# Performance work log

Hardware: AMD Instinct MI355X
Metric: run time of the kernel (lower is better)

Reference implementation:

```python
import jax, jax.numpy as jnp
import numpy as np

H = 8      # head_nums
D = 64     # head_planes
SCALE = D ** -0.5


def setup_inputs() -> dict:
    key = jax.random.key(0)
    ks = jax.random.split(key, 7)
    B, Nq, Nkv = 2, 2048, 2048
    Cq, Ck, I = 1024, 768, H * D
    return {
        "x": jax.random.normal(ks[0], (B, Nq, Cq), jnp.float32),
        "context": jax.random.normal(ks[1], (B, Nkv, Ck), jnp.float32),
        "Wq": jax.random.normal(ks[2], (Cq, I), jnp.float32) * (Cq ** -0.5),
        "Wk": jax.random.normal(ks[3], (Ck, I), jnp.float32) * (Ck ** -0.5),
        "Wv": jax.random.normal(ks[4], (Ck, I), jnp.float32) * (Ck ** -0.5),
        "Wo": jax.random.normal(ks[5], (I, Cq), jnp.float32) * (I ** -0.5),
        "bo": jnp.zeros((Cq,), jnp.float32),
    }


def reference(x, context, Wq, Wk, Wv, Wo, bo):
    B, Nq, _ = x.shape
    Nkv = context.shape[1]
    # projections (bias-free, as in to_q/to_k/to_v)
    q = (x @ Wq).reshape(B, Nq, H, D)        # b i h d
    k = (context @ Wk).reshape(B, Nkv, H, D)  # b j h d
    v = (context @ Wv).reshape(B, Nkv, H, D)
    # scaled dot-product attention, full [B,H,Nq,Nkv] scores as in original
    sim = jnp.einsum('bihd,bjhd->bhij', q, k) * SCALE
    attn = jax.nn.softmax(sim, axis=-1)
    out = jnp.einsum('bhij,bjhd->bihd', attn, v).reshape(B, Nq, H * D)
    # to_out linear (dropout_prob=0.0 -> identity)
    return out @ Wo + bo
```

## Files before the change

### kernel.cpp

```cpp
#include <hip/hip_runtime.h>
#include <hip/hip_bf16.h>

typedef __hip_bfloat16 bf16;
typedef __attribute__((ext_vector_type(8))) short short8;
typedef __attribute__((ext_vector_type(4))) float f32x4;

#define MFMA16(a, b, c) __builtin_amdgcn_mfma_f32_16x16x32_bf16((a), (b), (c), 0, 0, 0)

#define BATCH 2
#define NQ 2048
#define NKV 2048
#define HEADS 8
#define DHEAD 64
#define CQ 1024
#define CK 768
#define IDIM 512
#define SCALE 0.125f

__device__ __forceinline__ short8 ld8(const bf16* p) {
    return *(const short8*)p;
}

__device__ __forceinline__ void async_ld16(const bf16* g, bf16* l) {
    __builtin_amdgcn_global_load_lds((__attribute__((address_space(1))) const void*)g,
                                     (__attribute__((address_space(3))) void*)l,
                                     16, 0, 0);
}

__global__ __launch_bounds__(256) void prologue(
    const float* __restrict__ x, const float* __restrict__ ctx,
    const float* __restrict__ Wq, const float* __restrict__ Wk,
    const float* __restrict__ Wv, const float* __restrict__ Wo,
    bf16* __restrict__ Xb, bf16* __restrict__ Cb,
    bf16* __restrict__ WqT, bf16* __restrict__ WkT,
    bf16* __restrict__ WvT, bf16* __restrict__ WoT) {
    __shared__ float tile[64][65];
    const int t = threadIdx.x;
    const int bx = blockIdx.x;

    if (bx < 3584) {
        int idx = bx * 256 + t;
        const int NX8 = (4096 * 1024) / 8;
        const float4* srcp;
        bf16* dstp;
        if (idx < NX8) {
            srcp = (const float4*)x + (size_t)idx * 2;
            dstp = Xb + (size_t)idx * 8;
        } else {
            int j = idx - NX8;
            srcp = (const float4*)ctx + (size_t)j * 2;
            dstp = Cb + (size_t)j * 8;
        }
        float4 v0 = srcp[0], v1 = srcp[1];
        bf16 tmp[8] = {__float2bfloat16(v0.x), __float2bfloat16(v0.y),
                       __float2bfloat16(v0.z), __float2bfloat16(v0.w),
                       __float2bfloat16(v1.x), __float2bfloat16(v1.y),
                       __float2bfloat16(v1.z), __float2bfloat16(v1.w)};
        *(short8*)dstp = *(short8*)tmp;
        return;
    }

    int tb = bx - 3584;
    const float* src; bf16* dst; int R, C, ti;
    if (tb < 128)      { src = Wq; dst = WqT; R = 1024; C = 512;  ti = tb; }
    else if (tb < 224) { src = Wk; dst = WkT; R = 768;  C = 512;  ti = tb - 128; }
    else if (tb < 320) { src = Wv; dst = WvT; R = 768;  C = 512;  ti = tb - 224; }
    else               { src = Wo; dst = WoT; R = 512;  C = 1024; ti = tb - 320; }
    const int tilesC = C >> 6;
    const int tr = ti / tilesC, tc = ti - tr * tilesC;

    {
        int row = t >> 4;
        int c4 = (t & 15) * 4;
#pragma unroll
        for (int p = 0; p < 4; ++p) {
            float4 v = *(const float4*)&src[(size_t)(tr * 64 + p * 16 + row) * C + tc * 64 + c4];
            tile[p * 16 + row][c4 + 0] = v.x;
            tile[p * 16 + row][c4 + 1] = v.y;
            tile[p * 16 + row][c4 + 2] = v.z;
            tile[p * 16 + row][c4 + 3] = v.w;
        }
    }
    __syncthreads();
    {
        int oc = t >> 2;
        int r0 = (t & 3) * 16;
        bf16 tmp[16];
#pragma unroll
        for (int j = 0; j < 16; ++j)
            tmp[j] = __float2bfloat16(tile[r0 + j][oc]);
        bf16* dp = dst + (size_t)(tc * 64 + oc) * R + tr * 64 + r0;
        *(short8*)dp = *(short8*)&tmp[0];
        *(short8*)(dp + 8) = *(short8*)&tmp[8];
    }
}

__global__ __launch_bounds__(256) void qkv_gemm(
    const bf16* __restrict__ Xb, const bf16* __restrict__ Cb,
    const bf16* __restrict__ WqT, const bf16* __restrict__ WkT,
    const bf16* __restrict__ WvT,
    bf16* __restrict__ Qb, bf16* __restrict__ Kb, bf16* __restrict__ Vt) {
    __shared__ bf16 At[2][64 * 64];
    __shared__ bf16 Bts[2][128 * 64];

    const int z = blockIdx.z;
    const bf16* A  = (z == 0) ? Xb : Cb;
    const bf16* Bt = (z == 0) ? WqT : (z == 1) ? WkT : WvT;
    const int K = (z == 0) ? 1024 : 768;

    const int t = threadIdx.x;
    const int wave = t >> 6;
    const int lane = t & 63;
    const int n15 = lane & 15;
    const int quad = lane >> 4;
    const int wm = wave >> 1;
    const int wn = wave & 1;
    const int bm = blockIdx.y;
    const int bn = blockIdx.x;

    f32x4 acc[2][4] = {};

    const bf16* Ablk = A + (size_t)bm * 64 * K;
    const bf16* Bblk = Bt + (size_t)bn * 128 * K;

    int ar[2], ac[2], br[4], bc[4];
#pragma unroll
    for (int i = 0; i < 2; ++i) {
        int g = i * 256 + t;
        ar[i] = g >> 3; ac[i] = ((g & 7) ^ (ar[i] & 7)) * 8;
    }
#pragma unroll
    for (int i = 0; i < 4; ++i) {
        int g = i * 256 + t;
        br[i] = g >> 3; bc[i] = ((g & 7) ^ (br[i] & 7)) * 8;
    }

#pragma unroll
    for (int i = 0; i < 2; ++i)
        async_ld16(Ablk + ar[i] * K + ac[i], &At[0][(i * 256 + t) * 8]);
#pragma unroll
    for (int i = 0; i < 4; ++i)
        async_ld16(Bblk + br[i] * K + bc[i], &Bts[0][(i * 256 + t) * 8]);
    __syncthreads();

    for (int k0 = 0; k0 < K; k0 += 64) {
        const int p = (k0 >> 6) & 1;
        if (k0 + 64 < K) {
            const int q = p ^ 1;
            const int kn = k0 + 64;
#pragma unroll
            for (int i = 0; i < 2; ++i)
                async_ld16(Ablk + ar[i] * K + kn + ac[i], &At[q][(i * 256 + t) * 8]);
#pragma unroll
            for (int i = 0; i < 4; ++i)
                async_ld16(Bblk + br[i] * K + kn + bc[i], &Bts[q][(i * 256 + t) * 8]);
        }

#pragma unroll
        for (int kh = 0; kh < 2; ++kh) {
            short8 af[2], bfr[4];
#pragma unroll
            for (int mt = 0; mt < 2; ++mt) {
                int R = wm * 32 + mt * 16 + n15;
                af[mt] = ld8(&At[p][R * 64 + (((kh * 4 + quad) ^ (R & 7)) * 8)]);
            }
#pragma unroll
            for (int nt = 0; nt < 4; ++nt) {
                int R = wn * 64 + nt * 16 + n15;
                bfr[nt] = ld8(&Bts[p][R * 64 + (((kh * 4 + quad) ^ (R & 7)) * 8)]);
            }
#pragma unroll
            for (int mt = 0; mt < 2; ++mt)
#pragma unroll
                for (int nt = 0; nt < 4; ++nt)
                    acc[mt][nt] = MFMA16(af[mt], bfr[nt], acc[mt][nt]);
        }

        __syncthreads();
    }

    bf16* C = (z == 0) ? Qb : (z == 1) ? Kb : Vt;
#pragma unroll
    for (int mt = 0; mt < 2; ++mt) {
#pragma unroll
        for (int nt = 0; nt < 4; ++nt) {
            int col = bn * 128 + wn * 64 + nt * 16 + n15;
#pragma unroll
            for (int r = 0; r < 4; ++r) {
                int row = bm * 64 + wm * 32 + mt * 16 + quad * 4 + r;
                bf16 v = __float2bfloat16(acc[mt][nt][r]);
                if (z < 2) {
                    C[(size_t)row * 512 + col] = v;
                } else {
                    int b = row >> 11, j = row & 2047;
                    int h = col >> 6, d = col & 63;
                    C[(size_t)(((b << 3) + h) * 64 + d) * 2048 + j] = v;
                }
            }
        }
    }
}

__global__ __launch_bounds__(256) void out_gemm(const bf16* __restrict__ A,
                                                const bf16* __restrict__ Bt,
                                                const float* __restrict__ bias,
                                                float* __restrict__ C) {
    const int K = 512, N = 1024;
    __shared__ char SMEM[49152];
    bf16* At  = (bf16*)SMEM;
    bf16* Bts = (bf16*)(SMEM + 16384);
    float* Ep = (float*)SMEM;

    const int t = threadIdx.x;
    const int wave = t >> 6;
    const int lane = t & 63;
    const int n15 = lane & 15;
    const int quad = lane >> 4;
    const int wm = wave >> 1;
    const int wn = wave & 1;
    const int bm = blockIdx.y;
    const int bn = blockIdx.x;

    f32x4 acc[2][4] = {};

    const bf16* Ablk = A + (size_t)bm * 64 * K;
    const bf16* Bblk = Bt + (size_t)bn * 128 * K;

    int ar[2], ac[2], br[4], bc[4];
#pragma unroll
    for (int i = 0; i < 2; ++i) {
        int g = i * 256 + t;
        ar[i] = g >> 3; ac[i] = ((g & 7) ^ (ar[i] & 7)) * 8;
    }
#pragma unroll
    for (int i = 0; i < 4; ++i) {
        int g = i * 256 + t;
        br[i] = g >> 3; bc[i] = ((g & 7) ^ (br[i] & 7)) * 8;
    }

#pragma unroll
    for (int i = 0; i < 2; ++i)
        async_ld16(Ablk + ar[i] * K + ac[i], At + (i * 256 + t) * 8);
#pragma unroll
    for (int i = 0; i < 4; ++i)
        async_ld16(Bblk + br[i] * K + bc[i], Bts + (i * 256 + t) * 8);
    __syncthreads();

    for (int k0 = 0; k0 < K; k0 += 64) {
        const int p = (k0 >> 6) & 1;
        if (k0 + 64 < K) {
            const int q = p ^ 1;
            const int kn = k0 + 64;
#pragma unroll
            for (int i = 0; i < 2; ++i)
                async_ld16(Ablk + ar[i] * K + kn + ac[i], At + q * 4096 + (i * 256 + t) * 8);
#pragma unroll
            for (int i = 0; i < 4; ++i)
                async_ld16(Bblk + br[i] * K + kn + bc[i], Bts + q * 8192 + (i * 256 + t) * 8);
        }

#pragma unroll
        for (int kh = 0; kh < 2; ++kh) {
            short8 af[2], bfr[4];
#pragma unroll
            for (int mt = 0; mt < 2; ++mt) {
                int R = wm * 32 + mt * 16 + n15;
                af[mt] = ld8(At + p * 4096 + R * 64 + (((kh * 4 + quad) ^ (R & 7)) * 8));
            }
#pragma unroll
            for (int nt = 0; nt < 4; ++nt) {
                int R = wn * 64 + nt * 16 + n15;
                bfr[nt] = ld8(Bts + p * 8192 + R * 64 + (((kh * 4 + quad) ^ (R & 7)) * 8));
            }
#pragma unroll
            for (int mt = 0; mt < 2; ++mt)
#pragma unroll
                for (int nt = 0; nt < 4; ++nt)
                    acc[mt][nt] = MFMA16(af[mt], bfr[nt], acc[mt][nt]);
        }

        __syncthreads();
    }

#pragma unroll
    for (int mt = 0; mt < 2; ++mt)
#pragma unroll
        for (int nt = 0; nt < 4; ++nt) {
            int col = wn * 64 + nt * 16 + n15;
#pragma unroll
            for (int r = 0; r < 4; ++r) {
                int row = wm * 32 + mt * 16 + quad * 4 + r;
                Ep[row * 132 + col] = acc[mt][nt][r];
            }
        }
    __syncthreads();

#pragma unroll
    for (int i = 0; i < 8; ++i) {
        int f4 = i * 256 + t;
        int row = f4 >> 5;
        int c4 = (f4 & 31) * 4;
        float4 v = *(float4*)&Ep[row * 132 + c4];
        float4 bv = *(const float4*)&bias[bn * 128 + c4];
        v.x += bv.x; v.y += bv.y; v.z += bv.z; v.w += bv.w;
        *(float4*)&C[(size_t)(bm * 64 + row) * N + bn * 128 + c4] = v;
    }
}

__global__ __launch_bounds__(512, 1) void flash_attn(const bf16* __restrict__ Q,
                                                     const bf16* __restrict__ K,
                                                     const bf16* __restrict__ Vt,
                                                     bf16* __restrict__ O) {
    __shared__ bf16 Kt[2][64 * 64];
    __shared__ bf16 Vte[2][64 * 64];
    __shared__ bf16 Pa[8][16 * 72];
    __shared__ float Oc[4][64][16];
    __shared__ float Lc[4][16];

    const int t = threadIdx.x;
    const int wave = t >> 6;
    const int g = wave >> 1;
    const int khalf = wave & 1;
    const int lane = t & 63;
    const int n15 = lane & 15;
    const int quad = lane >> 4;

    const int L = blockIdx.x;
    const int bh = L & 15;
    const int b = bh >> 3, h = bh & 7;
    const int q0 = (L >> 4) * 64;
    const int qw = q0 + g * 16;

    const bf16* Qp = Q + ((size_t)(b * NQ + qw) * IDIM + h * DHEAD);
    const bf16* Kp = K + ((size_t)b * NKV * IDIM + h * DHEAD)
                       + (size_t)(khalf * 1024) * IDIM;
    const bf16* Vp = Vt + (size_t)((b * HEADS + h) * DHEAD) * NKV + khalf * 1024;
    bf16* Pw = Pa[wave];

    short8 qa0 = ld8(Qp + n15 * IDIM + quad * 8);
    short8 qa1 = ld8(Qp + n15 * IDIM + 32 + quad * 8);

    const int s0 = g * 128 + lane;
    const int s1 = s0 + 64;
    const int r0 = s0 >> 3, c0 = (s0 & 7) ^ (r0 & 7);
    const int r1 = s1 >> 3, c1 = (s1 & 7) ^ (r1 & 7);
    const bf16* kg0 = Kp + r0 * IDIM + c0 * 8;
    const bf16* kg1 = Kp + r1 * IDIM + c1 * 8;
    const bf16* vg0 = Vp + (size_t)r0 * NKV + c0 * 8;
    const bf16* vg1 = Vp + (size_t)r1 * NKV + c1 * 8;
    bf16* kl0 = &Kt[khalf][s0 * 8];
    bf16* kl1 = &Kt[khalf][s1 * 8];
    bf16* vl0 = &Vte[khalf][s0 * 8];
    bf16* vl1 = &Vte[khalf][s1 * 8];

    f32x4 o[4] = {};
    float lsum = 0.f;
    const int sw = n15 & 7;

    for (int key0 = 0; key0 < 1024; key0 += 64) {
        async_ld16(kg0 + (size_t)key0 * IDIM, kl0);
        async_ld16(kg1 + (size_t)key0 * IDIM, kl1);
        async_ld16(vg0 + key0, vl0);
        async_ld16(vg1 + key0, vl1);
        __syncthreads();

        f32x4 s[4] = {};
#pragma unroll
        for (int su = 0; su < 4; ++su) {
            const bf16* kr = &Kt[khalf][(su * 16 + n15) * 64];
            short8 ka0 = ld8(kr + ((quad ^ sw) * 8));
            short8 ka1 = ld8(kr + (((4 + quad) ^ sw) * 8));
            s[su] = MFMA16(ka0, qa0, s[su]);
            s[su] = MFMA16(ka1, qa1, s[su]);
        }

#pragma unroll
        for (int su = 0; su < 4; ++su) {
            float p0 = __expf(s[su][0] * SCALE);
            float p1 = __expf(s[su][1] * SCALE);
            float p2 = __expf(s[su][2] * SCALE);
            float p3 = __expf(s[su][3] * SCALE);
            lsum += (p0 + p1) + (p2 + p3);
            bf16 pk[4] = {__float2bfloat16(p0), __float2bfloat16(p1),
                          __float2bfloat16(p2), __float2bfloat16(p3)};
            *(uint2*)&Pw[n15 * 72 + su * 16 + quad * 4] = *(uint2*)pk;
        }
        asm volatile("s_waitcnt lgkmcnt(0)" ::: "memory");

        short8 pb0 = ld8(&Pw[n15 * 72 + quad * 8]);
        short8 pb1 = ld8(&Pw[n15 * 72 + 32 + quad * 8]);

#pragma unroll
        for (int d4 = 0; d4 < 4; ++d4) {
            const bf16* vr = &Vte[khalf][(d4 * 16 + n15) * 64];
            short8 va0 = ld8(vr + ((quad ^ sw) * 8));
            short8 va1 = ld8(vr + (((4 + quad) ^ sw) * 8));
            o[d4] = MFMA16(va0, pb0, o[d4]);
            o[d4] = MFMA16(va1, pb1, o[d4]);
        }
        __syncthreads();
    }

    lsum += __shfl_xor(lsum, 16, 64);
    lsum += __shfl_xor(lsum, 32, 64);

    if (khalf == 1) {
#pragma unroll
        for (int d4 = 0; d4 < 4; ++d4)
#pragma unroll
            for (int r = 0; r < 4; ++r)
                Oc[g][d4 * 16 + quad * 4 + r][n15] = o[d4][r];
        if (quad == 0) Lc[g][n15] = lsum;
    }
    __syncthreads();
    if (khalf == 0) {
        float lt = lsum + Lc[g][n15];
        float inv = 1.0f / lt;
#pragma unroll
        for (int d4 = 0; d4 < 4; ++d4) {
            bf16 pk[4];
#pragma unroll
            for (int r = 0; r < 4; ++r) {
                float v = o[d4][r] + Oc[g][d4 * 16 + quad * 4 + r][n15];
                pk[r] = __float2bfloat16(v * inv);
            }
            *(uint2*)&Pa[g][n15 * 72 + d4 * 16 + quad * 4] = *(uint2*)pk;
        }
    }
    __syncthreads();

    {
        int ql = t >> 3, seg = t & 7;
        const bf16* src = &Pa[ql >> 4][(ql & 15) * 72 + seg * 8];
        short8 a0 = ld8(src);
        bf16* dst = O + ((size_t)(b * NQ + q0 + ql) * IDIM + h * DHEAD + seg * 8);
        *(short8*)dst = a0;
    }
}

extern "C" void kernel_launch(void* const* d_in, const int* in_sizes, int n_in,
                              void* d_out, int out_size, void* d_ws, size_t ws_size,
                              hipStream_t stream) {
    (void)in_sizes; (void)n_in; (void)out_size; (void)ws_size;

    const float* x   = (const float*)d_in[0];
    const float* ctx = (const float*)d_in[1];
    const float* Wq  = (const float*)d_in[2];
    const float* Wk  = (const float*)d_in[3];
    const float* Wv  = (const float*)d_in[4];
    const float* Wo  = (const float*)d_in[5];
    const float* bo  = (const float*)d_in[6];
    float* out = (float*)d_out;

    char* ws = (char*)d_ws;
    bf16* Xb  = (bf16*)(ws + 0);
    bf16* Cb  = (bf16*)(ws + 8388608);
    bf16* WqT = (bf16*)(ws + 14680064);
    bf16* WkT = (bf16*)(ws + 15728640);
    bf16* WvT = (bf16*)(ws + 16515072);
    bf16* WoT = (bf16*)(ws + 17301504);
    bf16* Qb  = (bf16*)(ws + 18350080);
    bf16* Kb  = (bf16*)(ws + 22544384);
    bf16* Vt  = (bf16*)(ws + 26738688);
    bf16* Ob  = (bf16*)(ws + 30932992);

    prologue<<<4032, 256, 0, stream>>>(x, ctx, Wq, Wk, Wv, Wo,
                                       Xb, Cb, WqT, WkT, WvT, WoT);

    qkv_gemm<<<dim3(4, 64, 3), 256, 0, stream>>>(Xb, Cb, WqT, WkT, WvT, Qb, Kb, Vt);

    flash_attn<<<512, 512, 0, stream>>>(Qb, Kb, Vt, Ob);

    out_gemm<<<dim3(8, 64), 256, 0, stream>>>(Ob, WoT, bo, out);
}
```

Before: 146.7 us.

## Double-buffer K/V in attention, keep P in registers, stage QKV epilogue

```diff
diff --git a/kernel.cpp b/kernel.cpp
--- a/kernel.cpp
+++ b/kernel.cpp
@@ -3,6 +3,7 @@
 
 typedef __hip_bfloat16 bf16;
 typedef __attribute__((ext_vector_type(8))) short short8;
+typedef __attribute__((ext_vector_type(4))) short short4_;
 typedef __attribute__((ext_vector_type(4))) float f32x4;
 
 #define MFMA16(a, b, c) __builtin_amdgcn_mfma_f32_16x16x32_bf16((a), (b), (c), 0, 0, 0)
@@ -25,6 +26,13 @@
     __builtin_amdgcn_global_load_lds((__attribute__((address_space(1))) const void*)g,
                                      (__attribute__((address_space(3))) void*)l,
                                      16, 0, 0);
+}
+
+__device__ __forceinline__ unsigned int pk2(float a, float b) {
+    union { bf16 h[2]; unsigned int u; } x;
+    x.h[0] = __float2bfloat16(a);
+    x.h[1] = __float2bfloat16(b);
+    return x.u;
 }
 
 __global__ __launch_bounds__(256) void prologue(
@@ -100,8 +108,10 @@
     const bf16* __restrict__ WqT, const bf16* __restrict__ WkT,
     const bf16* __restrict__ WvT,
     bf16* __restrict__ Qb, bf16* __restrict__ Kb, bf16* __restrict__ Vt) {
-    __shared__ bf16 At[2][64 * 64];
-    __shared__ bf16 Bts[2][128 * 64];
+    __shared__ char SMEM[49152];
+    bf16* At  = (bf16*)SMEM;
+    bf16* Bts = (bf16*)(SMEM + 16384);
+    bf16* Ep  = (bf16*)SMEM;
 
     const int z = blockIdx.z;
     const bf16* A  = (z == 0) ? Xb : Cb;
@@ -137,10 +147,10 @@
 
 #pragma unroll
     for (int i = 0; i < 2; ++i)
-        async_ld16(Ablk + ar[i] * K + ac[i], &At[0][(i * 256 + t) * 8]);
+        async_ld16(Ablk + ar[i] * K + ac[i], At + (i * 256 + t) * 8);
 #pragma unroll
     for (int i = 0; i < 4; ++i)
-        async_ld16(Bblk + br[i] * K + bc[i], &Bts[0][(i * 256 + t) * 8]);
+        async_ld16(Bblk + br[i] * K + bc[i], Bts + (i * 256 + t) * 8);
     __syncthreads();
 
     for (int k0 = 0; k0 < K; k0 += 64) {
@@ -150,10 +160,10 @@
             const int kn = k0 + 64;
 #pragma unroll
             for (int i = 0; i < 2; ++i)
-                async_ld16(Ablk + ar[i] * K + kn + ac[i], &At[q][(i * 256 + t) * 8]);
+                async_ld16(Ablk + ar[i] * K + kn + ac[i], At + q * 4096 + (i * 256 + t) * 8);
 #pragma unroll
             for (int i = 0; i < 4; ++i)
-                async_ld16(Bblk + br[i] * K + kn + bc[i], &Bts[q][(i * 256 + t) * 8]);
+                async_ld16(Bblk + br[i] * K + kn + bc[i], Bts + q * 8192 + (i * 256 + t) * 8);
         }
 
 #pragma unroll
@@ -162,12 +172,12 @@
 #pragma unroll
             for (int mt = 0; mt < 2; ++mt) {
                 int R = wm * 32 + mt * 16 + n15;
-                af[mt] = ld8(&At[p][R * 64 + (((kh * 4 + quad) ^ (R & 7)) * 8)]);
+                af[mt] = ld8(At + p * 4096 + R * 64 + (((kh * 4 + quad) ^ (R & 7)) * 8));
             }
 #pragma unroll
             for (int nt = 0; nt < 4; ++nt) {
                 int R = wn * 64 + nt * 16 + n15;
-                bfr[nt] = ld8(&Bts[p][R * 64 + (((kh * 4 + quad) ^ (R & 7)) * 8)]);
+                bfr[nt] = ld8(Bts + p * 8192 + R * 64 + (((kh * 4 + quad) ^ (R & 7)) * 8));
             }
 #pragma unroll
             for (int mt = 0; mt < 2; ++mt)
@@ -179,24 +189,53 @@
         __syncthreads();
     }
 
+    if (z < 2) {
+#pragma unroll
+        for (int mt = 0; mt < 2; ++mt)
+#pragma unroll
+            for (int nt = 0; nt < 4; ++nt) {
+                int col = wn * 64 + nt * 16 + n15;
+#pragma unroll
+                for (int r = 0; r < 4; ++r) {
+                    int row = wm * 32 + mt * 16 + quad * 4 + r;
+                    Ep[row * 136 + col] = __float2bfloat16(acc[mt][nt][r]);
+                }
+            }
+    } else {
+#pragma unroll
+        for (int mt = 0; mt < 2; ++mt)
+#pragma unroll
+            for (int nt = 0; nt < 4; ++nt) {
+                int col = wn * 64 + nt * 16 + n15;
+#pragma unroll
+                for (int r = 0; r < 4; ++r) {
+                    int row = wm * 32 + mt * 16 + quad * 4 + r;
+                    Ep[col * 72 + row] = __float2bfloat16(acc[mt][nt][r]);
+                }
+            }
+    }
+    __syncthreads();
+
     bf16* C = (z == 0) ? Qb : (z == 1) ? Kb : Vt;
-#pragma unroll
-    for (int mt = 0; mt < 2; ++mt) {
-#pragma unroll
-        for (int nt = 0; nt < 4; ++nt) {
-            int col = bn * 128 + wn * 64 + nt * 16 + n15;
-#pragma unroll
-            for (int r = 0; r < 4; ++r) {
-                int row = bm * 64 + wm * 32 + mt * 16 + quad * 4 + r;
-                bf16 v = __float2bfloat16(acc[mt][nt][r]);
-                if (z < 2) {
-                    C[(size_t)row * 512 + col] = v;
-                } else {
-                    int b = row >> 11, j = row & 2047;
-                    int h = col >> 6, d = col & 63;
-                    C[(size_t)(((b << 3) + h) * 64 + d) * 2048 + j] = v;
-                }
-            }
+    if (z < 2) {
+#pragma unroll
+        for (int i = 0; i < 4; ++i) {
+            int idx = i * 256 + t;
+            int row = idx >> 4, seg = idx & 15;
+            short8 v = ld8(&Ep[row * 136 + seg * 8]);
+            *(short8*)&C[(size_t)(bm * 64 + row) * 512 + bn * 128 + seg * 8] = v;
+        }
+    } else {
+        const int bb = bm >> 5;
+#pragma unroll
+        for (int i = 0; i < 4; ++i) {
+            int idx = i * 256 + t;
+            int col = idx >> 3, seg = idx & 7;
+            int cg = bn * 128 + col;
+            int hh = cg >> 6, dd = cg & 63;
+            int jrow = (bm & 31) * 64 + seg * 8;
+            short8 v = ld8(&Ep[col * 72 + seg * 8]);
+            *(short8*)&C[(size_t)(((bb << 3) + hh) * 64 + dd) * 2048 + jrow] = v;
         }
     }
 }
@@ -307,15 +346,15 @@
     }
 }
 
-__global__ __launch_bounds__(512, 1) void flash_attn(const bf16* __restrict__ Q,
+__global__ __launch_bounds__(512, 4) void flash_attn(const bf16* __restrict__ Q,
                                                      const bf16* __restrict__ K,
                                                      const bf16* __restrict__ Vt,
                                                      bf16* __restrict__ O) {
-    __shared__ bf16 Kt[2][64 * 64];
-    __shared__ bf16 Vte[2][64 * 64];
-    __shared__ bf16 Pa[8][16 * 72];
-    __shared__ float Oc[4][64][16];
-    __shared__ float Lc[4][16];
+    __shared__ bf16 Kt[2][2][64 * 64];
+    __shared__ bf16 Vte[2][2][64 * 64];
+    float* Oc = (float*)&Kt[0][0][0];
+    float* Lc = (float*)((char*)&Kt[0][0][0] + 16384);
+    bf16*  Pe = &Vte[0][0][0];
 
     const int t = threadIdx.x;
     const int wave = t >> 6;
@@ -335,7 +374,6 @@
     const bf16* Kp = K + ((size_t)b * NKV * IDIM + h * DHEAD)
                        + (size_t)(khalf * 1024) * IDIM;
     const bf16* Vp = Vt + (size_t)((b * HEADS + h) * DHEAD) * NKV + khalf * 1024;
-    bf16* Pw = Pa[wave];
 
     short8 qa0 = ld8(Qp + n15 * IDIM + quad * 8);
     short8 qa1 = ld8(Qp + n15 * IDIM + 32 + quad * 8);
@@ -348,32 +386,41 @@
     const bf16* kg1 = Kp + r1 * IDIM + c1 * 8;
     const bf16* vg0 = Vp + (size_t)r0 * NKV + c0 * 8;
     const bf16* vg1 = Vp + (size_t)r1 * NKV + c1 * 8;
-    bf16* kl0 = &Kt[khalf][s0 * 8];
-    bf16* kl1 = &Kt[khalf][s1 * 8];
-    bf16* vl0 = &Vte[khalf][s0 * 8];
-    bf16* vl1 = &Vte[khalf][s1 * 8];
 
     f32x4 o[4] = {};
     float lsum = 0.f;
     const int sw = n15 & 7;
-
-    for (int key0 = 0; key0 < 1024; key0 += 64) {
-        async_ld16(kg0 + (size_t)key0 * IDIM, kl0);
-        async_ld16(kg1 + (size_t)key0 * IDIM, kl1);
-        async_ld16(vg0 + key0, vl0);
-        async_ld16(vg1 + key0, vl1);
+    const int qh = quad >> 1;
+    const int qb = (quad & 1) << 2;
+
+    async_ld16(kg0, &Kt[0][khalf][s0 * 8]);
+    async_ld16(kg1, &Kt[0][khalf][s1 * 8]);
+    async_ld16(vg0, &Vte[0][khalf][s0 * 8]);
+    async_ld16(vg1, &Vte[0][khalf][s1 * 8]);
+
+    for (int it = 0; it < 16; ++it) {
+        const int cur = it & 1;
+        asm volatile("s_waitcnt vmcnt(0)" ::: "memory");
         __syncthreads();
+        if (it < 15) {
+            const int kn = (it + 1) * 64;
+            async_ld16(kg0 + (size_t)kn * IDIM, &Kt[cur ^ 1][khalf][s0 * 8]);
+            async_ld16(kg1 + (size_t)kn * IDIM, &Kt[cur ^ 1][khalf][s1 * 8]);
+            async_ld16(vg0 + kn, &Vte[cur ^ 1][khalf][s0 * 8]);
+            async_ld16(vg1 + kn, &Vte[cur ^ 1][khalf][s1 * 8]);
+        }
 
         f32x4 s[4] = {};
 #pragma unroll
         for (int su = 0; su < 4; ++su) {
-            const bf16* kr = &Kt[khalf][(su * 16 + n15) * 64];
+            const bf16* kr = &Kt[cur][khalf][(su * 16 + n15) * 64];
             short8 ka0 = ld8(kr + ((quad ^ sw) * 8));
             short8 ka1 = ld8(kr + (((4 + quad) ^ sw) * 8));
             s[su] = MFMA16(ka0, qa0, s[su]);
             s[su] = MFMA16(ka1, qa1, s[su]);
         }
 
+        unsigned int w[4][2];
 #pragma unroll
         for (int su = 0; su < 4; ++su) {
             float p0 = __expf(s[su][0] * SCALE);
@@ -381,57 +428,59 @@
             float p2 = __expf(s[su][2] * SCALE);
             float p3 = __expf(s[su][3] * SCALE);
             lsum += (p0 + p1) + (p2 + p3);
-            bf16 pk[4] = {__float2bfloat16(p0), __float2bfloat16(p1),
-                          __float2bfloat16(p2), __float2bfloat16(p3)};
-            *(uint2*)&Pw[n15 * 72 + su * 16 + quad * 4] = *(uint2*)pk;
-        }
-        asm volatile("s_waitcnt lgkmcnt(0)" ::: "memory");
-
-        short8 pb0 = ld8(&Pw[n15 * 72 + quad * 8]);
-        short8 pb1 = ld8(&Pw[n15 * 72 + 32 + quad * 8]);
+            w[su][0] = pk2(p0, p1);
+            w[su][1] = pk2(p2, p3);
+        }
+        union { short8 v; unsigned int u[4]; } pb0, pb1;
+        pb0.u[0] = w[0][0]; pb0.u[1] = w[0][1]; pb0.u[2] = w[1][0]; pb0.u[3] = w[1][1];
+        pb1.u[0] = w[2][0]; pb1.u[1] = w[2][1]; pb1.u[2] = w[3][0]; pb1.u[3] = w[3][1];
 
 #pragma unroll
         for (int d4 = 0; d4 < 4; ++d4) {
-            const bf16* vr = &Vte[khalf][(d4 * 16 + n15) * 64];
-            short8 va0 = ld8(vr + ((quad ^ sw) * 8));
-            short8 va1 = ld8(vr + (((4 + quad) ^ sw) * 8));
-            o[d4] = MFMA16(va0, pb0, o[d4]);
-            o[d4] = MFMA16(va1, pb1, o[d4]);
-        }
-        __syncthreads();
+            const bf16* vr = &Vte[cur][khalf][(d4 * 16 + n15) * 64];
+            union { short8 v; short4_ hh[2]; } va0, va1;
+            va0.hh[0] = *(const short4_*)(vr + (((qh    ) ^ sw) << 3) + qb);
+            va0.hh[1] = *(const short4_*)(vr + (((qh | 2) ^ sw) << 3) + qb);
+            va1.hh[0] = *(const short4_*)(vr + (((qh | 4) ^ sw) << 3) + qb);
+            va1.hh[1] = *(const short4_*)(vr + (((qh | 6) ^ sw) << 3) + qb);
+            o[d4] = MFMA16(va0.v, pb0.v, o[d4]);
+            o[d4] = MFMA16(va1.v, pb1.v, o[d4]);
+        }
     }
 
     lsum += __shfl_xor(lsum, 16, 64);
     lsum += __shfl_xor(lsum, 32, 64);
 
+    __syncthreads();
+
     if (khalf == 1) {
 #pragma unroll
         for (int d4 = 0; d4 < 4; ++d4)
 #pragma unroll
             for (int r = 0; r < 4; ++r)
-                Oc[g][d4 * 16 + quad * 4 + r][n15] = o[d4][r];
-        if (quad == 0) Lc[g][n15] = lsum;
+                Oc[(g * 64 + d4 * 16 + quad * 4 + r) * 16 + n15] = o[d4][r];
+        if (quad == 0) Lc[g * 16 + n15] = lsum;
     }
     __syncthreads();
     if (khalf == 0) {
-        float lt = lsum + Lc[g][n15];
+        float lt = lsum + Lc[g * 16 + n15];
         float inv = 1.0f / lt;
 #pragma unroll
         for (int d4 = 0; d4 < 4; ++d4) {
             bf16 pk[4];
 #pragma unroll
             for (int r = 0; r < 4; ++r) {
-                float v = o[d4][r] + Oc[g][d4 * 16 + quad * 4 + r][n15];
+                float v = o[d4][r] + Oc[(g * 64 + d4 * 16 + quad * 4 + r) * 16 + n15];
                 pk[r] = __float2bfloat16(v * inv);
             }
-            *(uint2*)&Pa[g][n15 * 72 + d4 * 16 + quad * 4] = *(uint2*)pk;
+            *(uint2*)&Pe[g * (16 * 72) + n15 * 72 + d4 * 16 + quad * 4] = *(uint2*)pk;
         }
     }
     __syncthreads();
 
     {
         int ql = t >> 3, seg = t & 7;
-        const bf16* src = &Pa[ql >> 4][(ql & 15) * 72 + seg * 8];
+        const bf16* src = &Pe[(ql >> 4) * (16 * 72) + (ql & 15) * 72 + seg * 8];
         short8 a0 = ld8(src);
         bf16* dst = O + ((size_t)(b * NQ + q0 + ql) * IDIM + h * DHEAD + seg * 8);
         *(short8*)dst = a0;
```

Result: no change. 149.0 us (+1.6%).
